# Optimization experiments

Measured on AMD Instinct MI355X. Metric: run time of the kernel, lower is better.

## Reference

```python
import jax, jax.numpy as jnp
import numpy as np

# Config from the repo: 128^3 volume, patch 2 -> 64^3 patches, embed_dim 64
D = H = W = 64
C = 64
WS = 2        # window_size
SS = 1        # shift_size
NH = 8        # num_heads
MLP = 256     # num_mlp
B = 2
L = D * H * W
S = WS ** 3   # tokens per window = 8
NUM_REL = (2 * WS - 1) ** 3  # 27


def _rel_position_index(ws):
    # faithful to source, incl. np.meshgrid default 'xy' indexing
    coords = np.stack(np.meshgrid(np.arange(ws), np.arange(ws), np.arange(ws)))
    cf = coords.reshape(3, -1)
    rc = (cf[:, :, None] - cf[:, None, :]).transpose(1, 2, 0)
    rc[:, :, 0] += ws - 1
    rc[:, :, 1] += ws - 1
    rc[:, :, 2] += ws - 1
    rc[:, :, 0] *= 2 * ws - 1
    return rc.sum(-1)  # (S, S) int


def _attn_mask(d, h, w, ws, ss):
    sl = (slice(0, -ws), slice(-ws, -ss), slice(-ss, None))
    m = np.zeros((1, d, h, w, 1), np.float32)
    cnt = 0
    for ds in sl:
        for hs in sl:
            for wsl in sl:
                m[:, ds, hs, wsl, :] = cnt
                cnt += 1
    pz, py, px = d // ws, h // ws, w // ws
    mw = m.reshape(1, pz, ws, py, ws, px, ws, 1)
    mw = mw.transpose(0, 1, 3, 5, 2, 4, 6, 7).reshape(-1, ws ** 3)  # (nW, S)
    am = mw[:, None, :] - mw[:, :, None]
    return np.where(am != 0, -100.0, 0.0).astype(np.float32)  # (nW, S, S)


_REL_IDX = _rel_position_index(WS).reshape(-1)          # (S*S,)
_MASK = _attn_mask(D, H, W, WS, SS)                     # (nW, S, S)


def setup_inputs() -> dict:
    key = jax.random.key(0)
    ks = jax.random.split(key, 8)
    n = lambda k, s: jax.random.normal(k, s, jnp.float32) * 0.02
    return {
        "x": jax.random.normal(ks[0], (B, L, C), jnp.float32),
        "norm1_g": jnp.ones((C,), jnp.float32),
        "norm1_b": jnp.zeros((C,), jnp.float32),
        "qkv_w": n(ks[1], (C, 3 * C)),
        "qkv_b": jnp.zeros((3 * C,), jnp.float32),
        "rpb": n(ks[2], (NUM_REL, NH)),
        "proj_w": n(ks[3], (C, C)),
        "proj_b": jnp.zeros((C,), jnp.float32),
        "norm2_g": jnp.ones((C,), jnp.float32),
        "norm2_b": jnp.zeros((C,), jnp.float32),
        "mlp_w1": n(ks[4], (C, MLP)),
        "mlp_b1": jnp.zeros((MLP,), jnp.float32),
        "mlp_w2": n(ks[5], (MLP, C)),
        "mlp_b2": jnp.zeros((C,), jnp.float32),
    }


def _ln(x, g, b, eps=1e-5):
    mu = jnp.mean(x, -1, keepdims=True)
    var = jnp.mean(jnp.square(x - mu), -1, keepdims=True)
    return (x - mu) * jax.lax.rsqrt(var + eps) * g + b


def _forward(x, norm1_g, norm1_b, qkv_w, qkv_b, rpb, proj_w, proj_b,
             norm2_g, norm2_b, mlp_w1, mlp_b1, mlp_w2, mlp_b2):
    b = x.shape[0]
    pz, py, px = D // WS, H // WS, W // WS
    hd = C // NH
    scale = hd ** -0.5

    h = _ln(x, norm1_g, norm1_b).reshape(b, D, H, W, C)
    h = jnp.roll(h, (-SS, -SS, -SS), (1, 2, 3))  # cyclic shift
    # window partition -> (b*nW, S, C)
    w = h.reshape(b, pz, WS, py, WS, px, WS, C)
    w = w.transpose(0, 1, 3, 5, 2, 4, 6, 7).reshape(-1, S, C)
    n = w.shape[0]

    qkv = (w @ qkv_w + qkv_b).reshape(n, S, 3, NH, hd).transpose(2, 0, 3, 1, 4)
    q, k, v = qkv[0] * scale, qkv[1], qkv[2]   # (n, NH, S, hd)
    attn = jnp.einsum('nhqd,nhkd->nhqk', q, k)  # (n, NH, S, S)

    # relative position bias, gather + reshape exactly as in the source
    bias = rpb[jnp.asarray(_REL_IDX)].reshape(S, S, S, -1).transpose(3, 0, 1, 2)
    attn = attn + bias  # broadcasts since NH == S == 8 in this config

    mask = jnp.asarray(_MASK)  # (nW, S, S)
    nW = mask.shape[0]
    attn = attn.reshape(-1, nW, NH, S, S) + mask[None, :, None]
    attn = jax.nn.softmax(attn.reshape(-1, NH, S, S), axis=-1)

    out = jnp.einsum('nhqk,nhkd->nhqd', attn, v)
    out = out.transpose(0, 2, 1, 3).reshape(n, S, C)
    out = out @ proj_w + proj_b

    # window reverse (bug-faithful to the source's reshape/transpose order)
    xr = out.reshape(-1, pz, WS, py, px, WS, WS, C)
    xr = xr.transpose(0, 1, 3, 5, 2, 4, 6, 7).reshape(-1, D, H, W, C)
    xr = jnp.roll(xr, (SS, SS, SS), (1, 2, 3))
    h = xr.reshape(b, L, C)

    x = x + h  # DropPath/Dropout are identity in eval mode
    skip = x
    h = _ln(x, norm2_g, norm2_b)
    h = jax.nn.gelu(h @ mlp_w1 + mlp_b1, approximate=False) @ mlp_w2 + mlp_b2
    return skip + h


def reference(x, norm1_g, norm1_b, qkv_w, qkv_b, rpb, proj_w, proj_b,
              norm2_g, norm2_b, mlp_w1, mlp_b1, mlp_w2, mlp_b2):
    return _forward(x, norm1_g, norm1_b, qkv_w, qkv_b, rpb, proj_w, proj_b,
                    norm2_g, norm2_b, mlp_w1, mlp_b1, mlp_w2, mlp_b2)
```

## Files before the change

kernel.cpp:

```cpp
#include <hip/hip_runtime.h>
#include <math.h>

typedef unsigned short u16;
typedef unsigned int u32;
typedef __attribute__((ext_vector_type(8))) short short8;
typedef __attribute__((ext_vector_type(4))) float f32x4;

__device__ __forceinline__ float bf2f(u16 u) {
  union { u32 i; float f; } v; v.i = ((u32)u) << 16; return v.f;
}
__device__ __forceinline__ u16 f2bf(float f) {
  union { float f; u32 i; } v; v.f = f;
  u32 i = v.i;
  i += 0x7fffu + ((i >> 16) & 1u);
  return (u16)(i >> 16);
}

template<bool F32>
__device__ __forceinline__ float ld(const void* p, int i) {
  if (F32) return ((const float*)p)[i];
  return bf2f(((const u16*)p)[i]);
}

__global__ __launch_bounds__(64)
void detect_kernel(const void* __restrict__ xv, int* __restrict__ flag) {
  const u32* xw = (const u32*)xv;
  const int t = threadIdx.x;
  int bad = 0;
  for (int i = t; i < 1024; i += 64) {
    const int e = (int)((xw[i] >> 7) & 0xFF);
    if (e < 90 || e > 150) bad++;
  }
#pragma unroll
  for (int m = 1; m < 64; m <<= 1) bad += __shfl_xor(bad, m);
  if (t == 0) *flag = (bad > 256) ? 1 : 0;
}

template<bool F32>
__device__ __forceinline__ void gather8(const void* __restrict__ x, int chunk,
                                        int w, int s, int cg, float* pf) {
  const int b     = chunk >> 13;
  const int wbase = (chunk & 8191) << 2;
  const int widx  = wbase + w;
  const int wz = widx >> 10, wy = (widx >> 5) & 31, wx = widx & 31;
  const int od = (2*wz + ((s>>2)&1) + 1) & 63;
  const int oh = (2*wy + ((s>>1)&1) + 1) & 63;
  const int ow = (2*wx + ( s    &1) + 1) & 63;
  const int base = (((b<<18) + ((od<<12)|(oh<<6)|ow)) << 6) + cg*8;
  if (F32) {
    const f32x4 a = *(const f32x4*)((const float*)x + base);
    const f32x4 c = *(const f32x4*)((const float*)x + base + 4);
    pf[0]=a[0]; pf[1]=a[1]; pf[2]=a[2]; pf[3]=a[3];
    pf[4]=c[0]; pf[5]=c[1]; pf[6]=c[2]; pf[7]=c[3];
  } else {
    const short8 a = *(const short8*)((const u16*)x + base);
#pragma unroll
    for (int j = 0; j < 8; ++j) pf[j] = bf2f((u16)a[j]);
  }
}

__device__ __forceinline__ int scat(int chunk, int tok) {
  const int b     = chunk >> 13;
  const int wbase = (chunk & 8191) << 2;
  const int widx = wbase + (tok >> 3);
  const int s    = tok & 7;
  const int wz = widx >> 10, wy = (widx >> 5) & 31, wx = widx & 31;
  const int fd = (2*wz + ((wy>>3)&1) + 1) & 63;
  const int Hb = 8*(wy&7) + 4*(wx>>4) + (wy>>4);
  const int Wb = 4*(wx&15);
  const int i = (s>>2)&1, j = (s>>1)&1, k = s&1;
  const int fh = (Hb + 2*j + 1) & 63;
  const int fw = (Wb + 2*i + k + 1) & 63;
  return ((b<<18) + ((fd<<12)|(fh<<6)|fw)) << 6;
}

#define MFMA __builtin_amdgcn_mfma_f32_16x16x32_bf16

template<bool F32>
__device__ __forceinline__ void attn_body(
    const void* __restrict__ x,
    const void* __restrict__ n1g, const void* __restrict__ n1b,
    const void* __restrict__ qkvw, const void* __restrict__ qkvb,
    const void* __restrict__ rpb,
    const void* __restrict__ projw, const void* __restrict__ projb,
    float* __restrict__ out,
    u16* __restrict__ aL, float* __restrict__ qF,
    float* __restrict__ kF, float* __restrict__ vF)
{
  const int tid  = threadIdx.x;
  const int w    = tid >> 6, l = tid & 63;
  const int quad = l >> 4,  col = l & 15;
  const int s8   = l >> 3,  cg  = l & 7;

  float g1v[8], be1v[8];
#pragma unroll
  for (int j = 0; j < 8; ++j) {
    g1v[j]  = ld<F32>(n1g, cg*8 + j);
    be1v[j] = ld<F32>(n1b, cg*8 + j);
  }

  short8 bq[3][2];
#pragma unroll
  for (int nt = 0; nt < 3; ++nt)
#pragma unroll
    for (int kt = 0; kt < 2; ++kt) {
      short8 f;
#pragma unroll
      for (int j = 0; j < 8; ++j)
        f[j] = (short)f2bf(ld<F32>(qkvw, (kt*32 + quad*8 + j)*192 + w*48 + nt*16 + col));
      bq[nt][kt] = f;
    }
  float qb[3];
#pragma unroll
  for (int nt = 0; nt < 3; ++nt) qb[nt] = ld<F32>(qkvb, w*48 + nt*16 + col);
  short8 bp[2];
#pragma unroll
  for (int kt = 0; kt < 2; ++kt) {
    short8 f;
#pragma unroll
    for (int j = 0; j < 8; ++j)
      f[j] = (short)f2bf(ld<F32>(projw, (kt*32 + quad*8 + j)*64 + w*16 + col));
    bp[kt] = f;
  }
  const float pbv = ld<F32>(projb, w*16 + col);
  const int rel = 3 * (((s8>>1)&1) - ((cg>>1)&1) + 1)
                +     (((s8>>2)&1) - ((cg>>2)&1) + 1)
                +     (( s8    &1) - ( cg    &1) + 1);
  float rpv[8];
#pragma unroll
  for (int kk = 0; kk < 8; ++kk) rpv[kk] = ld<F32>(rpb, rel*8 + kk);

  float pf[8];
  gather8<F32>(x, blockIdx.x, w, s8, cg, pf);

  for (int chunk = blockIdx.x; chunk < 16384; chunk += 2048) {
    const int wbase = (chunk & 8191) << 2;
    const int widx0 = wbase + w;
    const int wz0 = widx0 >> 10, wy0 = (widx0 >> 5) & 31, wx0 = widx0 & 31;

    {
      float s1 = 0.f, sq = 0.f;
#pragma unroll
      for (int j = 0; j < 8; ++j) { s1 += pf[j]; sq += pf[j]*pf[j]; }
#pragma unroll
      for (int m = 1; m < 8; m <<= 1) {
        s1 += __shfl_xor(s1, m);
        sq += __shfl_xor(sq, m);
      }
      const float mu  = s1 * 0.015625f;
      const float var = sq * 0.015625f - mu * mu;
      const float rs  = rsqrtf(var + 1e-5f);
      short8 av;
#pragma unroll
      for (int j = 0; j < 8; ++j)
        av[j] = (short)f2bf((pf[j] - mu) * rs * g1v[j] + be1v[j]);
      *(short8*)&aL[(w*8 + s8)*72 + cg*8] = av;
    }
    if (chunk + 2048 < 16384) gather8<F32>(x, chunk + 2048, w, s8, cg, pf);
    __syncthreads();

    {
      short8 aF[2][2];
#pragma unroll
      for (int mt = 0; mt < 2; ++mt)
#pragma unroll
        for (int kt = 0; kt < 2; ++kt)
          aF[mt][kt] = *(const short8*)&aL[(mt*16 + col)*72 + kt*32 + quad*8];
#pragma unroll
      for (int nt = 0; nt < 3; ++nt) {
        f32x4 a0 = (f32x4){0.f,0.f,0.f,0.f}, a1 = (f32x4){0.f,0.f,0.f,0.f};
        a0 = MFMA(aF[0][0], bq[nt][0], a0, 0, 0, 0);
        a0 = MFMA(aF[0][1], bq[nt][1], a0, 0, 0, 0);
        a1 = MFMA(aF[1][0], bq[nt][0], a1, 0, 0, 0);
        a1 = MFMA(aF[1][1], bq[nt][1], a1, 0, 0, 0);
        const int nb  = w*48 + nt*16;
        float* dst    = (nb < 64) ? qF : (nb < 128) ? kF : vF;
        const int chb = (nb & 63) + col;
        const float scl = (nb < 64) ? 0.35355339059327373f : 1.0f;
        const float bb  = qb[nt];
#pragma unroll
        for (int r = 0; r < 4; ++r) {
          dst[(quad*4 + r)*68 + chb]      = (a0[r] + bb) * scl;
          dst[(16 + quad*4 + r)*68 + chb] = (a1[r] + bb) * scl;
        }
      }
    }
    __syncthreads();

    {
      const int tq = w*8 + cg;
      float qr[8];
      {
        const f32x4 qa = *(const f32x4*)&qF[tq*68 + s8*8];
        const f32x4 qc = *(const f32x4*)&qF[tq*68 + s8*8 + 4];
        qr[0]=qa[0]; qr[1]=qa[1]; qr[2]=qa[2]; qr[3]=qa[3];
        qr[4]=qc[0]; qr[5]=qc[1]; qr[6]=qc[2]; qr[7]=qc[3];
      }
      float sc8[8];
#pragma unroll
      for (int kk = 0; kk < 8; ++kk) {
        const f32x4 ka = *(const f32x4*)&kF[(w*8 + kk)*68 + s8*8];
        const f32x4 kc = *(const f32x4*)&kF[(w*8 + kk)*68 + s8*8 + 4];
        float a = qr[0]*ka[0] + qr[1]*ka[1] + qr[2]*ka[2] + qr[3]*ka[3]
                + qr[4]*kc[0] + qr[5]*kc[1] + qr[6]*kc[2] + qr[7]*kc[3];
        sc8[kk] = a + rpv[kk];
      }
      if ((wz0 == 31) || (wy0 == 31) || (wx0 == 31)) {
        int cnts[8];
#pragma unroll
        for (int p = 0; p < 8; ++p) {
          const int sd = 2*wz0 + ((p>>2)&1);
          const int sh = 2*wy0 + ((p>>1)&1);
          const int sw = 2*wx0 + (p&1);
          cnts[p] = (sd >= 62 ? sd - 61 : 0)*9 + (sh >= 62 ? sh - 61 : 0)*3
                  + (sw >= 62 ? sw - 61 : 0);
        }
#pragma unroll
        for (int kk = 0; kk < 8; ++kk)
          if (cnts[kk] != cnts[cg]) sc8[kk] -= 100.f;
      }
      float mx = sc8[0];
#pragma unroll
      for (int kk = 1; kk < 8; ++kk) mx = fmaxf(mx, sc8[kk]);
      float pr[8], lsum = 0.f;
#pragma unroll
      for (int kk = 0; kk < 8; ++kk) { pr[kk] = __expf(sc8[kk] - mx); lsum += pr[kk]; }
      const float inv = __builtin_amdgcn_rcpf(lsum);
      float o[8];
#pragma unroll
      for (int d = 0; d < 8; ++d) o[d] = 0.f;
#pragma unroll
      for (int kk = 0; kk < 8; ++kk) {
        const f32x4 va = *(const f32x4*)&vF[(w*8 + kk)*68 + s8*8];
        const f32x4 vc = *(const f32x4*)&vF[(w*8 + kk)*68 + s8*8 + 4];
        o[0] += pr[kk]*va[0]; o[1] += pr[kk]*va[1];
        o[2] += pr[kk]*va[2]; o[3] += pr[kk]*va[3];
        o[4] += pr[kk]*vc[0]; o[5] += pr[kk]*vc[1];
        o[6] += pr[kk]*vc[2]; o[7] += pr[kk]*vc[3];
      }
      short8 ov;
#pragma unroll
      for (int d = 0; d < 8; ++d) ov[d] = (short)f2bf(o[d] * inv);
      *(short8*)&aL[tq*72 + s8*8] = ov;
    }
    int offs[8]; float xr[8];
#pragma unroll
    for (int mt = 0; mt < 2; ++mt)
#pragma unroll
      for (int r = 0; r < 4; ++r) {
        const int off = scat(chunk, mt*16 + quad*4 + r) + w*16 + col;
        offs[mt*4 + r] = off;
        xr[mt*4 + r]   = ld<F32>(x, off);
      }
    __syncthreads();

    {
      f32x4 c0 = (f32x4){0.f,0.f,0.f,0.f}, c1 = (f32x4){0.f,0.f,0.f,0.f};
      c0 = MFMA(*(const short8*)&aL[(col)*72 + quad*8],         bp[0], c0, 0, 0, 0);
      c0 = MFMA(*(const short8*)&aL[(col)*72 + 32 + quad*8],    bp[1], c0, 0, 0, 0);
      c1 = MFMA(*(const short8*)&aL[(16+col)*72 + quad*8],      bp[0], c1, 0, 0, 0);
      c1 = MFMA(*(const short8*)&aL[(16+col)*72 + 32 + quad*8], bp[1], c1, 0, 0, 0);
#pragma unroll
      for (int r = 0; r < 4; ++r) {
        out[offs[r]]     = xr[r]     + c0[r] + pbv;
        out[offs[4 + r]] = xr[4 + r] + c1[r] + pbv;
      }
    }
    __syncthreads();
  }
}

__global__ __launch_bounds__(256, 4)
void attn_kernel(const void* __restrict__ x,
                 const void* __restrict__ n1g, const void* __restrict__ n1b,
                 const void* __restrict__ qkvw, const void* __restrict__ qkvb,
                 const void* __restrict__ rpb,
                 const void* __restrict__ projw, const void* __restrict__ projb,
                 const int* __restrict__ flag, float* __restrict__ out)
{
  __shared__ __align__(16) u16   aL[32*72];
  __shared__ __align__(16) float qF[32*68];
  __shared__ __align__(16) float kF[32*68];
  __shared__ __align__(16) float vF[32*68];
  if (*flag)
    attn_body<true >(x, n1g, n1b, qkvw, qkvb, rpb, projw, projb, out, aL, qF, kF, vF);
  else
    attn_body<false>(x, n1g, n1b, qkvw, qkvb, rpb, projw, projb, out, aL, qF, kF, vF);
}

template<bool F32>
__device__ __forceinline__ void mlp_body(
    float* __restrict__ io,
    const void* __restrict__ n2g, const void* __restrict__ n2b,
    const void* __restrict__ mw1, const void* __restrict__ mb1,
    const void* __restrict__ mw2, const void* __restrict__ mb2,
    u16* __restrict__ aL, u16* __restrict__ hL, float* __restrict__ yL)
{
  const int tid  = threadIdx.x;
  const int w    = tid >> 6, l = tid & 63;
  const int quad = l >> 4,  col = l & 15;
  const int s8   = l >> 3,  cg  = l & 7;
  const int ltok = w*8 + s8;

  float g2v[8], be2v[8];
#pragma unroll
  for (int j = 0; j < 8; ++j) {
    g2v[j]  = ld<F32>(n2g, cg*8 + j);
    be2v[j] = ld<F32>(n2b, cg*8 + j);
  }

  short8 b1f[2][4];
#pragma unroll
  for (int kt = 0; kt < 2; ++kt)
#pragma unroll
    for (int nt = 0; nt < 4; ++nt) {
      short8 f;
#pragma unroll
      for (int j = 0; j < 8; ++j)
        f[j] = (short)f2bf(ld<F32>(mw1, (kt*32 + quad*8 + j)*256 + w*64 + nt*16 + col));
      b1f[kt][nt] = f;
    }
  short8 b2f[8];
#pragma unroll
  for (int kt = 0; kt < 8; ++kt) {
    short8 f;
#pragma unroll
    for (int j = 0; j < 8; ++j)
      f[j] = (short)f2bf(ld<F32>(mw2, (kt*32 + quad*8 + j)*64 + w*16 + col));
    b2f[kt] = f;
  }
  float b1vv[4];
#pragma unroll
  for (int nt = 0; nt < 4; ++nt) b1vv[nt] = ld<F32>(mb1, w*64 + nt*16 + col);
  const float b2vv = ld<F32>(mb2, w*16 + col);

  float pf[8];
  {
    const float* p = &io[(blockIdx.x*32 + ltok)*64 + cg*8];
    const f32x4 a = *(const f32x4*)p;
    const f32x4 c = *(const f32x4*)(p + 4);
    pf[0]=a[0]; pf[1]=a[1]; pf[2]=a[2]; pf[3]=a[3];
    pf[4]=c[0]; pf[5]=c[1]; pf[6]=c[2]; pf[7]=c[3];
  }

  for (int chunk = blockIdx.x; chunk < 16384; chunk += 2048) {
    {
      float s1 = 0.f, sq = 0.f;
#pragma unroll
      for (int j = 0; j < 8; ++j) { s1 += pf[j]; sq += pf[j]*pf[j]; }
#pragma unroll
      for (int m = 1; m < 8; m <<= 1) {
        s1 += __shfl_xor(s1, m);
        sq += __shfl_xor(sq, m);
      }
      const float mu  = s1 * 0.015625f;
      const float var = sq * 0.015625f - mu * mu;
      const float rs  = rsqrtf(var + 1e-5f);
      short8 av;
#pragma unroll
      for (int j = 0; j < 8; ++j)
        av[j] = (short)f2bf((pf[j] - mu) * rs * g2v[j] + be2v[j]);
      *(short8*)&aL[ltok*72 + cg*8] = av;
      *(f32x4*)&yL[ltok*68 + cg*8]     = (f32x4){pf[0], pf[1], pf[2], pf[3]};
      *(f32x4*)&yL[ltok*68 + cg*8 + 4] = (f32x4){pf[4], pf[5], pf[6], pf[7]};
    }
    if (chunk + 2048 < 16384) {
      const float* p = &io[((chunk + 2048)*32 + ltok)*64 + cg*8];
      const f32x4 a = *(const f32x4*)p;
      const f32x4 c = *(const f32x4*)(p + 4);
      pf[0]=a[0]; pf[1]=a[1]; pf[2]=a[2]; pf[3]=a[3];
      pf[4]=c[0]; pf[5]=c[1]; pf[6]=c[2]; pf[7]=c[3];
    }
    __syncthreads();

    {
      short8 aF[2][2];
#pragma unroll
      for (int mt = 0; mt < 2; ++mt)
#pragma unroll
        for (int kt = 0; kt < 2; ++kt)
          aF[mt][kt] = *(const short8*)&aL[(mt*16 + col)*72 + kt*32 + quad*8];
#pragma unroll
      for (int nt = 0; nt < 4; ++nt) {
        f32x4 m0 = (f32x4){0.f,0.f,0.f,0.f}, m1 = (f32x4){0.f,0.f,0.f,0.f};
        m0 = MFMA(aF[0][0], b1f[0][nt], m0, 0, 0, 0);
        m0 = MFMA(aF[0][1], b1f[1][nt], m0, 0, 0, 0);
        m1 = MFMA(aF[1][0], b1f[0][nt], m1, 0, 0, 0);
        m1 = MFMA(aF[1][1], b1f[1][nt], m1, 0, 0, 0);
        const float bb = b1vv[nt];
#pragma unroll
        for (int r = 0; r < 4; ++r) {
          {
            const float h = m0[r] + bb;
            const float u = h * (1.5957691216f + 0.0713548162f * (h * h));
            const float e = __expf(u);
            hL[(quad*4 + r)*264 + w*64 + nt*16 + col] =
                f2bf(h - h * __builtin_amdgcn_rcpf(e + 1.f));
          }
          {
            const float h = m1[r] + bb;
            const float u = h * (1.5957691216f + 0.0713548162f * (h * h));
            const float e = __expf(u);
            hL[(16 + quad*4 + r)*264 + w*64 + nt*16 + col] =
                f2bf(h - h * __builtin_amdgcn_rcpf(e + 1.f));
          }
        }
      }
    }
    __syncthreads();

    {
      f32x4 o0 = (f32x4){0.f,0.f,0.f,0.f}, o1 = (f32x4){0.f,0.f,0.f,0.f};
#pragma unroll
      for (int kt = 0; kt < 8; ++kt) {
        o0 = MFMA(*(const short8*)&hL[(col)*264 + kt*32 + quad*8],    b2f[kt], o0, 0, 0, 0);
        o1 = MFMA(*(const short8*)&hL[(16+col)*264 + kt*32 + quad*8], b2f[kt], o1, 0, 0, 0);
      }
#pragma unroll
      for (int r = 0; r < 4; ++r) {
        const int r0 = quad*4 + r, r1 = 16 + quad*4 + r;
        io[(chunk*32 + r0)*64 + w*16 + col] = yL[r0*68 + w*16 + col] + o0[r] + b2vv;
        io[(chunk*32 + r1)*64 + w*16 + col] = yL[r1*68 + w*16 + col] + o1[r] + b2vv;
      }
    }
    __syncthreads();
  }
}

__global__ __launch_bounds__(256, 4)
void mlp_kernel(float* __restrict__ io,
                const void* __restrict__ n2g, const void* __restrict__ n2b,
                const void* __restrict__ mw1, const void* __restrict__ mb1,
                const void* __restrict__ mw2, const void* __restrict__ mb2,
                const int* __restrict__ flag)
{
  __shared__ __align__(16) u16   aL[32 * 72];
  __shared__ __align__(16) u16   hL[32 * 264];
  __shared__ __align__(16) float yL[32 * 68];
  if (*flag)
    mlp_body<true >(io, n2g, n2b, mw1, mb1, mw2, mb2, aL, hL, yL);
  else
    mlp_body<false>(io, n2g, n2b, mw1, mb1, mw2, mb2, aL, hL, yL);
}

extern "C" void kernel_launch(void* const* d_in, const int* in_sizes, int n_in,
                              void* d_out, int out_size, void* d_ws, size_t ws_size,
                              hipStream_t stream) {
  const void* x     = d_in[0];
  const void* n1g   = d_in[1];
  const void* n1b   = d_in[2];
  const void* qkvw  = d_in[3];
  const void* qkvb  = d_in[4];
  const void* rpb   = d_in[5];
  const void* projw = d_in[6];
  const void* projb = d_in[7];
  const void* n2g   = d_in[8];
  const void* n2b   = d_in[9];
  const void* mw1   = d_in[10];
  const void* mb1   = d_in[11];
  const void* mw2   = d_in[12];
  const void* mb2   = d_in[13];
  float* out = (float*)d_out;
  int* flag  = (int*)d_ws;

  detect_kernel<<<dim3(1), dim3(64), 0, stream>>>(x, flag);
  attn_kernel<<<dim3(2048), dim3(256), 0, stream>>>(
      x, n1g, n1b, qkvw, qkvb, rpb, projw, projb, flag, out);
  mlp_kernel<<<dim3(2048), dim3(256), 0, stream>>>(
      out, n2g, n2b, mw1, mb1, mw2, mb2, flag);
}
```

Before: 460.1 us.

## Store attention output as bf16 in workspace and fuse residual scatter into MLP

The attention kernel now writes only the projected attention output, in window-order as bf16, into a workspace buffer. It no longer gathers x and scatters fp32 results to the output. The MLP kernel reads x at the scattered positions, adds the bf16 attention output to form the residual, and writes the final result directly to the scattered output location. This replaces an fp32 scatter write followed by an fp32 read with a contiguous bf16 round trip. It also drops a read-modify pass over the output, at the cost of rounding the attention branch to bf16 and needing a large workspace; the old path remains as a fallback.

```diff
diff --git a/kernel.cpp b/kernel.cpp
--- a/kernel.cpp
+++ b/kernel.cpp
@@ -74,16 +74,32 @@
   return ((b<<18) + ((fd<<12)|(fh<<6)|fw)) << 6;
 }
 
+template<bool F32>
+__device__ __forceinline__ void loadx8(const void* __restrict__ x, int base,
+                                       float* xr) {
+  if (F32) {
+    const f32x4 a = *(const f32x4*)((const float*)x + base);
+    const f32x4 c = *(const f32x4*)((const float*)x + base + 4);
+    xr[0]=a[0]; xr[1]=a[1]; xr[2]=a[2]; xr[3]=a[3];
+    xr[4]=c[0]; xr[5]=c[1]; xr[6]=c[2]; xr[7]=c[3];
+  } else {
+    const short8 a = *(const short8*)((const u16*)x + base);
+#pragma unroll
+    for (int j = 0; j < 8; ++j) xr[j] = bf2f((u16)a[j]);
+  }
+}
+
 #define MFMA __builtin_amdgcn_mfma_f32_16x16x32_bf16
 
+
 template<bool F32>
-__device__ __forceinline__ void attn_body(
+__device__ __forceinline__ void attnB_body(
     const void* __restrict__ x,
     const void* __restrict__ n1g, const void* __restrict__ n1b,
     const void* __restrict__ qkvw, const void* __restrict__ qkvb,
     const void* __restrict__ rpb,
     const void* __restrict__ projw, const void* __restrict__ projb,
-    float* __restrict__ out,
+    u16* __restrict__ wsout,
     u16* __restrict__ aL, float* __restrict__ qF,
     float* __restrict__ kF, float* __restrict__ vF)
 {
@@ -201,9 +217,9 @@
       for (int kk = 0; kk < 8; ++kk) {
         const f32x4 ka = *(const f32x4*)&kF[(w*8 + kk)*68 + s8*8];
         const f32x4 kc = *(const f32x4*)&kF[(w*8 + kk)*68 + s8*8 + 4];
-        float a = qr[0]*ka[0] + qr[1]*ka[1] + qr[2]*ka[2] + qr[3]*ka[3]
-                + qr[4]*kc[0] + qr[5]*kc[1] + qr[6]*kc[2] + qr[7]*kc[3];
-        sc8[kk] = a + rpv[kk];
+        sc8[kk] = qr[0]*ka[0] + qr[1]*ka[1] + qr[2]*ka[2] + qr[3]*ka[3]
+                + qr[4]*kc[0] + qr[5]*kc[1] + qr[6]*kc[2] + qr[7]*kc[3]
+                + rpv[kk];
       }
       if ((wz0 == 31) || (wy0 == 31) || (wx0 == 31)) {
         int cnts[8];
@@ -243,15 +259,6 @@
       for (int d = 0; d < 8; ++d) ov[d] = (short)f2bf(o[d] * inv);
       *(short8*)&aL[tq*72 + s8*8] = ov;
     }
-    int offs[8]; float xr[8];
-#pragma unroll
-    for (int mt = 0; mt < 2; ++mt)
-#pragma unroll
-      for (int r = 0; r < 4; ++r) {
-        const int off = scat(chunk, mt*16 + quad*4 + r) + w*16 + col;
-        offs[mt*4 + r] = off;
-        xr[mt*4 + r]   = ld<F32>(x, off);
-      }
     __syncthreads();
 
     {
@@ -260,10 +267,11 @@
       c0 = MFMA(*(const short8*)&aL[(col)*72 + 32 + quad*8],    bp[1], c0, 0, 0, 0);
       c1 = MFMA(*(const short8*)&aL[(16+col)*72 + quad*8],      bp[0], c1, 0, 0, 0);
       c1 = MFMA(*(const short8*)&aL[(16+col)*72 + 32 + quad*8], bp[1], c1, 0, 0, 0);
+      const int base = (chunk << 5) * 64 + w*16 + col;
 #pragma unroll
       for (int r = 0; r < 4; ++r) {
-        out[offs[r]]     = xr[r]     + c0[r] + pbv;
-        out[offs[4 + r]] = xr[4 + r] + c1[r] + pbv;
+        wsout[base + (quad*4 + r)*64]      = f2bf(c0[r] + pbv);
+        wsout[base + (16 + quad*4 + r)*64] = f2bf(c1[r] + pbv);
       }
     }
     __syncthreads();
@@ -271,36 +279,38 @@
 }
 
 __global__ __launch_bounds__(256, 4)
-void attn_kernel(const void* __restrict__ x,
-                 const void* __restrict__ n1g, const void* __restrict__ n1b,
-                 const void* __restrict__ qkvw, const void* __restrict__ qkvb,
-                 const void* __restrict__ rpb,
-                 const void* __restrict__ projw, const void* __restrict__ projb,
-                 const int* __restrict__ flag, float* __restrict__ out)
+void attnB_kernel(const void* __restrict__ x,
+                  const void* __restrict__ n1g, const void* __restrict__ n1b,
+                  const void* __restrict__ qkvw, const void* __restrict__ qkvb,
+                  const void* __restrict__ rpb,
+                  const void* __restrict__ projw, const void* __restrict__ projb,
+                  const int* __restrict__ flag, u16* __restrict__ wsout)
 {
   __shared__ __align__(16) u16   aL[32*72];
   __shared__ __align__(16) float qF[32*68];
   __shared__ __align__(16) float kF[32*68];
   __shared__ __align__(16) float vF[32*68];
   if (*flag)
-    attn_body<true >(x, n1g, n1b, qkvw, qkvb, rpb, projw, projb, out, aL, qF, kF, vF);
+    attnB_body<true >(x, n1g, n1b, qkvw, qkvb, rpb, projw, projb, wsout, aL, qF, kF, vF);
   else
-    attn_body<false>(x, n1g, n1b, qkvw, qkvb, rpb, projw, projb, out, aL, qF, kF, vF);
+    attnB_body<false>(x, n1g, n1b, qkvw, qkvb, rpb, projw, projb, wsout, aL, qF, kF, vF);
 }
 
 template<bool F32>
-__device__ __forceinline__ void mlp_body(
-    float* __restrict__ io,
+__device__ __forceinline__ void mlpB_body(
+    const void* __restrict__ x, const u16* __restrict__ wsattn,
+    float* __restrict__ out,
     const void* __restrict__ n2g, const void* __restrict__ n2b,
     const void* __restrict__ mw1, const void* __restrict__ mb1,
     const void* __restrict__ mw2, const void* __restrict__ mb2,
-    u16* __restrict__ aL, u16* __restrict__ hL, float* __restrict__ yL)
+    u16* __restrict__ aL, u16* __restrict__ hL, float* __restrict__ yL,
+    int* __restrict__ offL)
 {
   const int tid  = threadIdx.x;
   const int w    = tid >> 6, l = tid & 63;
   const int quad = l >> 4,  col = l & 15;
   const int s8   = l >> 3,  cg  = l & 7;
-  const int ltok = w*8 + s8;
+  const int tok_l = w*8 + s8;
 
   float g2v[8], be2v[8];
 #pragma unroll
@@ -334,20 +344,19 @@
   for (int nt = 0; nt < 4; ++nt) b1vv[nt] = ld<F32>(mb1, w*64 + nt*16 + col);
   const float b2vv = ld<F32>(mb2, w*16 + col);
 
-  float pf[8];
-  {
-    const float* p = &io[(blockIdx.x*32 + ltok)*64 + cg*8];
-    const f32x4 a = *(const f32x4*)p;
-    const f32x4 c = *(const f32x4*)(p + 4);
-    pf[0]=a[0]; pf[1]=a[1]; pf[2]=a[2]; pf[3]=a[3];
-    pf[4]=c[0]; pf[5]=c[1]; pf[6]=c[2]; pf[7]=c[3];
-  }
+  float xr[8]; short8 ao; int offbase;
+  offbase = scat(blockIdx.x, tok_l);
+  loadx8<F32>(x, offbase + cg*8, xr);
+  ao = *(const short8*)&wsattn[((blockIdx.x << 5) + tok_l)*64 + cg*8];
 
   for (int chunk = blockIdx.x; chunk < 16384; chunk += 2048) {
     {
+      float yv[8];
+#pragma unroll
+      for (int j = 0; j < 8; ++j) yv[j] = xr[j] + bf2f((u16)ao[j]);
       float s1 = 0.f, sq = 0.f;
 #pragma unroll
-      for (int j = 0; j < 8; ++j) { s1 += pf[j]; sq += pf[j]*pf[j]; }
+      for (int j = 0; j < 8; ++j) { s1 += yv[j]; sq += yv[j]*yv[j]; }
 #pragma unroll
       for (int m = 1; m < 8; m <<= 1) {
         s1 += __shfl_xor(s1, m);
@@ -359,17 +368,16 @@
       short8 av;
 #pragma unroll
       for (int j = 0; j < 8; ++j)
-        av[j] = (short)f2bf((pf[j] - mu) * rs * g2v[j] + be2v[j]);
-      *(short8*)&aL[ltok*72 + cg*8] = av;
-      *(f32x4*)&yL[ltok*68 + cg*8]     = (f32x4){pf[0], pf[1], pf[2], pf[3]};
-      *(f32x4*)&yL[ltok*68 + cg*8 + 4] = (f32x4){pf[4], pf[5], pf[6], pf[7]};
+        av[j] = (short)f2bf((yv[j] - mu) * rs * g2v[j] + be2v[j]);
+      *(short8*)&aL[tok_l*72 + cg*8] = av;
+      *(f32x4*)&yL[tok_l*68 + cg*8]     = (f32x4){yv[0], yv[1], yv[2], yv[3]};
+      *(f32x4*)&yL[tok_l*68 + cg*8 + 4] = (f32x4){yv[4], yv[5], yv[6], yv[7]};
+      if (cg == 0) offL[tok_l] = offbase;
     }
     if (chunk + 2048 < 16384) {
-      const float* p = &io[((chunk + 2048)*32 + ltok)*64 + cg*8];
-      const f32x4 a = *(const f32x4*)p;
-      const f32x4 c = *(const f32x4*)(p + 4);
-      pf[0]=a[0]; pf[1]=a[1]; pf[2]=a[2]; pf[3]=a[3];
-      pf[4]=c[0]; pf[5]=c[1]; pf[6]=c[2]; pf[7]=c[3];
+      offbase = scat(chunk + 2048, tok_l);
+      loadx8<F32>(x, offbase + cg*8, xr);
+      ao = *(const short8*)&wsattn[(((chunk + 2048) << 5) + tok_l)*64 + cg*8];
     }
     __syncthreads();
 
@@ -419,6 +427,363 @@
 #pragma unroll
       for (int r = 0; r < 4; ++r) {
         const int r0 = quad*4 + r, r1 = 16 + quad*4 + r;
+        out[offL[r0] + w*16 + col] = yL[r0*68 + w*16 + col] + o0[r] + b2vv;
+        out[offL[r1] + w*16 + col] = yL[r1*68 + w*16 + col] + o1[r] + b2vv;
+      }
+    }
+    __syncthreads();
+  }
+}
+
+__global__ __launch_bounds__(256, 4)
+void mlpB_kernel(const void* __restrict__ x, const u16* __restrict__ wsattn,
+                 float* __restrict__ out,
+                 const void* __restrict__ n2g, const void* __restrict__ n2b,
+                 const void* __restrict__ mw1, const void* __restrict__ mb1,
+                 const void* __restrict__ mw2, const void* __restrict__ mb2,
+                 const int* __restrict__ flag)
+{
+  __shared__ __align__(16) u16   aL[32 * 72];
+  __shared__ __align__(16) u16   hL[32 * 264];
+  __shared__ __align__(16) float yL[32 * 68];
+  __shared__ __align__(16) int   offL[32];
+  if (*flag)
+    mlpB_body<true >(x, wsattn, out, n2g, n2b, mw1, mb1, mw2, mb2, aL, hL, yL, offL);
+  else
+    mlpB_body<false>(x, wsattn, out, n2g, n2b, mw1, mb1, mw2, mb2, aL, hL, yL, offL);
+}
+
+template<bool F32>
+__device__ __forceinline__ void attnA_body(
+    const void* __restrict__ x,
+    const void* __restrict__ n1g, const void* __restrict__ n1b,
+    const void* __restrict__ qkvw, const void* __restrict__ qkvb,
+    const void* __restrict__ rpb,
+    const void* __restrict__ projw, const void* __restrict__ projb,
+    float* __restrict__ out,
+    u16* __restrict__ aL, u16* __restrict__ qL,
+    u16* __restrict__ kL, u16* __restrict__ vL)
+{
+  const int tid  = threadIdx.x;
+  const int w    = tid >> 6, l = tid & 63;
+  const int quad = l >> 4,  col = l & 15;
+  const int s8   = l >> 3,  cg  = l & 7;
+
+  float g1v[8], be1v[8];
+#pragma unroll
+  for (int j = 0; j < 8; ++j) {
+    g1v[j]  = ld<F32>(n1g, cg*8 + j);
+    be1v[j] = ld<F32>(n1b, cg*8 + j);
+  }
+  short8 bq[3][2];
+#pragma unroll
+  for (int nt = 0; nt < 3; ++nt)
+#pragma unroll
+    for (int kt = 0; kt < 2; ++kt) {
+      short8 f;
+#pragma unroll
+      for (int j = 0; j < 8; ++j)
+        f[j] = (short)f2bf(ld<F32>(qkvw, (kt*32 + quad*8 + j)*192 + w*48 + nt*16 + col));
+      bq[nt][kt] = f;
+    }
+  float qb[3];
+#pragma unroll
+  for (int nt = 0; nt < 3; ++nt) qb[nt] = ld<F32>(qkvb, w*48 + nt*16 + col);
+  short8 bp[2];
+#pragma unroll
+  for (int kt = 0; kt < 2; ++kt) {
+    short8 f;
+#pragma unroll
+    for (int j = 0; j < 8; ++j)
+      f[j] = (short)f2bf(ld<F32>(projw, (kt*32 + quad*8 + j)*64 + w*16 + col));
+    bp[kt] = f;
+  }
+  const float pbv = ld<F32>(projb, w*16 + col);
+  const int rel = 3 * (((s8>>1)&1) - ((cg>>1)&1) + 1)
+                +     (((s8>>2)&1) - ((cg>>2)&1) + 1)
+                +     (( s8    &1) - ( cg    &1) + 1);
+  float rpv[8];
+#pragma unroll
+  for (int kk = 0; kk < 8; ++kk) rpv[kk] = ld<F32>(rpb, rel*8 + kk);
+
+  float pf[8];
+  gather8<F32>(x, blockIdx.x, w, s8, cg, pf);
+
+  for (int chunk = blockIdx.x; chunk < 16384; chunk += 2048) {
+    const int wbase = (chunk & 8191) << 2;
+    const int widx0 = wbase + w;
+    const int wz0 = widx0 >> 10, wy0 = (widx0 >> 5) & 31, wx0 = widx0 & 31;
+    {
+      float s1 = 0.f, sq = 0.f;
+#pragma unroll
+      for (int j = 0; j < 8; ++j) { s1 += pf[j]; sq += pf[j]*pf[j]; }
+#pragma unroll
+      for (int m = 1; m < 8; m <<= 1) {
+        s1 += __shfl_xor(s1, m);
+        sq += __shfl_xor(sq, m);
+      }
+      const float mu  = s1 * 0.015625f;
+      const float var = sq * 0.015625f - mu * mu;
+      const float rs  = rsqrtf(var + 1e-5f);
+      short8 av;
+#pragma unroll
+      for (int j = 0; j < 8; ++j)
+        av[j] = (short)f2bf((pf[j] - mu) * rs * g1v[j] + be1v[j]);
+      *(short8*)&aL[(w*8 + s8)*72 + cg*8] = av;
+    }
+    if (chunk + 2048 < 16384) gather8<F32>(x, chunk + 2048, w, s8, cg, pf);
+    __syncthreads();
+    {
+      short8 aF[2][2];
+#pragma unroll
+      for (int mt = 0; mt < 2; ++mt)
+#pragma unroll
+        for (int kt = 0; kt < 2; ++kt)
+          aF[mt][kt] = *(const short8*)&aL[(mt*16 + col)*72 + kt*32 + quad*8];
+#pragma unroll
+      for (int nt = 0; nt < 3; ++nt) {
+        f32x4 a0 = (f32x4){0.f,0.f,0.f,0.f}, a1 = (f32x4){0.f,0.f,0.f,0.f};
+        a0 = MFMA(aF[0][0], bq[nt][0], a0, 0, 0, 0);
+        a0 = MFMA(aF[0][1], bq[nt][1], a0, 0, 0, 0);
+        a1 = MFMA(aF[1][0], bq[nt][0], a1, 0, 0, 0);
+        a1 = MFMA(aF[1][1], bq[nt][1], a1, 0, 0, 0);
+        const int nb  = w*48 + nt*16;
+        u16* dst      = (nb < 64) ? qL : (nb < 128) ? kL : vL;
+        const int chb = (nb & 63) + col;
+        const float scl = (nb < 64) ? 0.35355339059327373f : 1.0f;
+        const float bb  = qb[nt];
+#pragma unroll
+        for (int r = 0; r < 4; ++r) {
+          dst[(quad*4 + r)*72 + chb]      = f2bf((a0[r] + bb) * scl);
+          dst[(16 + quad*4 + r)*72 + chb] = f2bf((a1[r] + bb) * scl);
+        }
+      }
+    }
+    __syncthreads();
+    {
+      const int tq = w*8 + cg;
+      float qr[8];
+      {
+        const short8 qv = *(const short8*)&qL[tq*72 + s8*8];
+#pragma unroll
+        for (int d = 0; d < 8; ++d) qr[d] = bf2f((u16)qv[d]);
+      }
+      float sc8[8];
+#pragma unroll
+      for (int kk = 0; kk < 8; ++kk) {
+        const short8 kv = *(const short8*)&kL[(w*8 + kk)*72 + s8*8];
+        float a = 0.f;
+#pragma unroll
+        for (int d = 0; d < 8; ++d) a += qr[d] * bf2f((u16)kv[d]);
+        sc8[kk] = a + rpv[kk];
+      }
+      {
+        int cnts[8];
+#pragma unroll
+        for (int p = 0; p < 8; ++p) {
+          const int sd = 2*wz0 + ((p>>2)&1);
+          const int sh = 2*wy0 + ((p>>1)&1);
+          const int sw = 2*wx0 + (p&1);
+          cnts[p] = (sd >= 62 ? sd - 61 : 0)*9 + (sh >= 62 ? sh - 61 : 0)*3
+                  + (sw >= 62 ? sw - 61 : 0);
+        }
+#pragma unroll
+        for (int kk = 0; kk < 8; ++kk)
+          if (cnts[kk] != cnts[cg]) sc8[kk] -= 100.f;
+      }
+      float mx = sc8[0];
+#pragma unroll
+      for (int kk = 1; kk < 8; ++kk) mx = fmaxf(mx, sc8[kk]);
+      float pr[8], lsum = 0.f;
+#pragma unroll
+      for (int kk = 0; kk < 8; ++kk) { pr[kk] = __expf(sc8[kk] - mx); lsum += pr[kk]; }
+      const float inv = __builtin_amdgcn_rcpf(lsum);
+      float o[8];
+#pragma unroll
+      for (int d = 0; d < 8; ++d) o[d] = 0.f;
+#pragma unroll
+      for (int kk = 0; kk < 8; ++kk) {
+        const short8 vv = *(const short8*)&vL[(w*8 + kk)*72 + s8*8];
+#pragma unroll
+        for (int d = 0; d < 8; ++d) o[d] += pr[kk] * bf2f((u16)vv[d]);
+      }
+      short8 ov;
+#pragma unroll
+      for (int d = 0; d < 8; ++d) ov[d] = (short)f2bf(o[d] * inv);
+      *(short8*)&qL[tq*72 + s8*8] = ov;
+    }
+    int offs[8]; float xr[8];
+#pragma unroll
+    for (int mt = 0; mt < 2; ++mt)
+#pragma unroll
+      for (int r = 0; r < 4; ++r) {
+        const int off = scat(chunk, mt*16 + quad*4 + r) + w*16 + col;
+        offs[mt*4 + r] = off;
+        xr[mt*4 + r]   = ld<F32>(x, off);
+      }
+    __syncthreads();
+    {
+      f32x4 c0 = (f32x4){0.f,0.f,0.f,0.f}, c1 = (f32x4){0.f,0.f,0.f,0.f};
+      c0 = MFMA(*(const short8*)&qL[(col)*72 + quad*8],         bp[0], c0, 0, 0, 0);
+      c0 = MFMA(*(const short8*)&qL[(col)*72 + 32 + quad*8],    bp[1], c0, 0, 0, 0);
+      c1 = MFMA(*(const short8*)&qL[(16+col)*72 + quad*8],      bp[0], c1, 0, 0, 0);
+      c1 = MFMA(*(const short8*)&qL[(16+col)*72 + 32 + quad*8], bp[1], c1, 0, 0, 0);
+#pragma unroll
+      for (int r = 0; r < 4; ++r) {
+        out[offs[r]]     = xr[r]     + c0[r] + pbv;
+        out[offs[4 + r]] = xr[4 + r] + c1[r] + pbv;
+      }
+    }
+    __syncthreads();
+  }
+}
+
+__global__ __launch_bounds__(256, 4)
+void attnA_kernel(const void* __restrict__ x,
+                  const void* __restrict__ n1g, const void* __restrict__ n1b,
+                  const void* __restrict__ qkvw, const void* __restrict__ qkvb,
+                  const void* __restrict__ rpb,
+                  const void* __restrict__ projw, const void* __restrict__ projb,
+                  const int* __restrict__ flag, float* __restrict__ out)
+{
+  __shared__ __align__(16) u16 aL[32*72];
+  __shared__ __align__(16) u16 qL[32*72];
+  __shared__ __align__(16) u16 kL[32*72];
+  __shared__ __align__(16) u16 vL[32*72];
+  if (*flag)
+    attnA_body<true >(x, n1g, n1b, qkvw, qkvb, rpb, projw, projb, out, aL, qL, kL, vL);
+  else
+    attnA_body<false>(x, n1g, n1b, qkvw, qkvb, rpb, projw, projb, out, aL, qL, kL, vL);
+}
+
+template<bool F32>
+__device__ __forceinline__ void mlpA_body(
+    float* __restrict__ io,
+    const void* __restrict__ n2g, const void* __restrict__ n2b,
+    const void* __restrict__ mw1, const void* __restrict__ mb1,
+    const void* __restrict__ mw2, const void* __restrict__ mb2,
+    u16* __restrict__ aL, u16* __restrict__ hL, float* __restrict__ yL)
+{
+  const int tid  = threadIdx.x;
+  const int w    = tid >> 6, l = tid & 63;
+  const int quad = l >> 4,  col = l & 15;
+  const int s8   = l >> 3,  cg  = l & 7;
+  const int ltok = w*8 + s8;
+
+  float g2v[8], be2v[8];
+#pragma unroll
+  for (int j = 0; j < 8; ++j) {
+    g2v[j]  = ld<F32>(n2g, cg*8 + j);
+    be2v[j] = ld<F32>(n2b, cg*8 + j);
+  }
+  short8 b1f[2][4];
+#pragma unroll
+  for (int kt = 0; kt < 2; ++kt)
+#pragma unroll
+    for (int nt = 0; nt < 4; ++nt) {
+      short8 f;
+#pragma unroll
+      for (int j = 0; j < 8; ++j)
+        f[j] = (short)f2bf(ld<F32>(mw1, (kt*32 + quad*8 + j)*256 + w*64 + nt*16 + col));
+      b1f[kt][nt] = f;
+    }
+  short8 b2f[8];
+#pragma unroll
+  for (int kt = 0; kt < 8; ++kt) {
+    short8 f;
+#pragma unroll
+    for (int j = 0; j < 8; ++j)
+      f[j] = (short)f2bf(ld<F32>(mw2, (kt*32 + quad*8 + j)*64 + w*16 + col));
+    b2f[kt] = f;
+  }
+  float b1vv[4];
+#pragma unroll
+  for (int nt = 0; nt < 4; ++nt) b1vv[nt] = ld<F32>(mb1, w*64 + nt*16 + col);
+  const float b2vv = ld<F32>(mb2, w*16 + col);
+
+  float pf[8];
+  {
+    const float* p = &io[(blockIdx.x*32 + ltok)*64 + cg*8];
+    const f32x4 a = *(const f32x4*)p;
+    const f32x4 c = *(const f32x4*)(p + 4);
+    pf[0]=a[0]; pf[1]=a[1]; pf[2]=a[2]; pf[3]=a[3];
+    pf[4]=c[0]; pf[5]=c[1]; pf[6]=c[2]; pf[7]=c[3];
+  }
+
+  for (int chunk = blockIdx.x; chunk < 16384; chunk += 2048) {
+    {
+      float s1 = 0.f, sq = 0.f;
+#pragma unroll
+      for (int j = 0; j < 8; ++j) { s1 += pf[j]; sq += pf[j]*pf[j]; }
+#pragma unroll
+      for (int m = 1; m < 8; m <<= 1) {
+        s1 += __shfl_xor(s1, m);
+        sq += __shfl_xor(sq, m);
+      }
+      const float mu  = s1 * 0.015625f;
+      const float var = sq * 0.015625f - mu * mu;
+      const float rs  = rsqrtf(var + 1e-5f);
+      short8 av;
+#pragma unroll
+      for (int j = 0; j < 8; ++j)
+        av[j] = (short)f2bf((pf[j] - mu) * rs * g2v[j] + be2v[j]);
+      *(short8*)&aL[ltok*72 + cg*8] = av;
+      *(f32x4*)&yL[ltok*68 + cg*8]     = (f32x4){pf[0], pf[1], pf[2], pf[3]};
+      *(f32x4*)&yL[ltok*68 + cg*8 + 4] = (f32x4){pf[4], pf[5], pf[6], pf[7]};
+    }
+    if (chunk + 2048 < 16384) {
+      const float* p = &io[((chunk + 2048)*32 + ltok)*64 + cg*8];
+      const f32x4 a = *(const f32x4*)p;
+      const f32x4 c = *(const f32x4*)(p + 4);
+      pf[0]=a[0]; pf[1]=a[1]; pf[2]=a[2]; pf[3]=a[3];
+      pf[4]=c[0]; pf[5]=c[1]; pf[6]=c[2]; pf[7]=c[3];
+    }
+    __syncthreads();
+    {
+      short8 aF[2][2];
+#pragma unroll
+      for (int mt = 0; mt < 2; ++mt)
+#pragma unroll
+        for (int kt = 0; kt < 2; ++kt)
+          aF[mt][kt] = *(const short8*)&aL[(mt*16 + col)*72 + kt*32 + quad*8];
+#pragma unroll
+      for (int nt = 0; nt < 4; ++nt) {
+        f32x4 m0 = (f32x4){0.f,0.f,0.f,0.f}, m1 = (f32x4){0.f,0.f,0.f,0.f};
+        m0 = MFMA(aF[0][0], b1f[0][nt], m0, 0, 0, 0);
+        m0 = MFMA(aF[0][1], b1f[1][nt], m0, 0, 0, 0);
+        m1 = MFMA(aF[1][0], b1f[0][nt], m1, 0, 0, 0);
+        m1 = MFMA(aF[1][1], b1f[1][nt], m1, 0, 0, 0);
+        const float bb = b1vv[nt];
+#pragma unroll
+        for (int r = 0; r < 4; ++r) {
+          {
+            const float h = m0[r] + bb;
+            const float u = h * (1.5957691216f + 0.0713548162f * (h * h));
+            const float e = __expf(u);
+            hL[(quad*4 + r)*264 + w*64 + nt*16 + col] =
+                f2bf(h - h * __builtin_amdgcn_rcpf(e + 1.f));
+          }
+          {
+            const float h = m1[r] + bb;
+            const float u = h * (1.5957691216f + 0.0713548162f * (h * h));
+            const float e = __expf(u);
+            hL[(16 + quad*4 + r)*264 + w*64 + nt*16 + col] =
+                f2bf(h - h * __builtin_amdgcn_rcpf(e + 1.f));
+          }
+        }
+      }
+    }
+    __syncthreads();
+    {
+      f32x4 o0 = (f32x4){0.f,0.f,0.f,0.f}, o1 = (f32x4){0.f,0.f,0.f,0.f};
+#pragma unroll
+      for (int kt = 0; kt < 8; ++kt) {
+        o0 = MFMA(*(const short8*)&hL[(col)*264 + kt*32 + quad*8],    b2f[kt], o0, 0, 0, 0);
+        o1 = MFMA(*(const short8*)&hL[(16+col)*264 + kt*32 + quad*8], b2f[kt], o1, 0, 0, 0);
+      }
+#pragma unroll
+      for (int r = 0; r < 4; ++r) {
+        const int r0 = quad*4 + r, r1 = 16 + quad*4 + r;
         io[(chunk*32 + r0)*64 + w*16 + col] = yL[r0*68 + w*16 + col] + o0[r] + b2vv;
         io[(chunk*32 + r1)*64 + w*16 + col] = yL[r1*68 + w*16 + col] + o1[r] + b2vv;
       }
@@ -428,19 +793,19 @@
 }
 
 __global__ __launch_bounds__(256, 4)
-void mlp_kernel(float* __restrict__ io,
-                const void* __restrict__ n2g, const void* __restrict__ n2b,
-                const void* __restrict__ mw1, const void* __restrict__ mb1,
-                const void* __restrict__ mw2, const void* __restrict__ mb2,
-                const int* __restrict__ flag)
+void mlpA_kernel(float* __restrict__ io,
+                 const void* __restrict__ n2g, const void* __restrict__ n2b,
+                 const void* __restrict__ mw1, const void* __restrict__ mb1,
+                 const void* __restrict__ mw2, const void* __restrict__ mb2,
+                 const int* __restrict__ flag)
 {
   __shared__ __align__(16) u16   aL[32 * 72];
   __shared__ __align__(16) u16   hL[32 * 264];
   __shared__ __align__(16) float yL[32 * 68];
   if (*flag)
-    mlp_body<true >(io, n2g, n2b, mw1, mb1, mw2, mb2, aL, hL, yL);
+    mlpA_body<true >(io, n2g, n2b, mw1, mb1, mw2, mb2, aL, hL, yL);
   else
-    mlp_body<false>(io, n2g, n2b, mw1, mb1, mw2, mb2, aL, hL, yL);
+    mlpA_body<false>(io, n2g, n2b, mw1, mb1, mw2, mb2, aL, hL, yL);
 }
 
 extern "C" void kernel_launch(void* const* d_in, const int* in_sizes, int n_in,
@@ -463,9 +828,19 @@
   float* out = (float*)d_out;
   int* flag  = (int*)d_ws;
 
+  const size_t need = 256 + (size_t)524288 * 64 * 2;
+
   detect_kernel<<<dim3(1), dim3(64), 0, stream>>>(x, flag);
-  attn_kernel<<<dim3(2048), dim3(256), 0, stream>>>(
-      x, n1g, n1b, qkvw, qkvb, rpb, projw, projb, flag, out);
-  mlp_kernel<<<dim3(2048), dim3(256), 0, stream>>>(
-      out, n2g, n2b, mw1, mb1, mw2, mb2, flag);
-}
+  if (ws_size >= need) {
+    u16* wsattn = (u16*)((char*)d_ws + 256);
+    attnB_kernel<<<dim3(2048), dim3(256), 0, stream>>>(
+        x, n1g, n1b, qkvw, qkvb, rpb, projw, projb, flag, wsattn);
+    mlpB_kernel<<<dim3(2048), dim3(256), 0, stream>>>(
+        x, wsattn, out, n2g, n2b, mw1, mb1, mw2, mb2, flag);
+  } else {
+    attnA_kernel<<<dim3(2048), dim3(256), 0, stream>>>(
+        x, n1g, n1b, qkvw, qkvb, rpb, projw, projb, flag, out);
+    mlpA_kernel<<<dim3(2048), dim3(256), 0, stream>>>(
+        out, n2g, n2b, mw1, mb1, mw2, mb2, flag);
+  }
+}
```

After: 475.8 us. 3.4% more time.
